# Kernel tuning notes

Measured on AMD Instinct MI355X. Metric: run time of the kernel, lower is better.

The kernel has to match this reference:

```python
import jax, jax.numpy as jnp
import numpy as np

PS = 32
EMBED_DIM = 768
IN_CH = 3
IMG = 1024
NUM_PATCHES = 992  # ini_row = i for H=1024, so need i+32 <= 1024
SPIKE_IDX = np.array([5, 300, 800])
SPIKE_VAL = 1.0e6  # makes val ~= 23.94 < 24 -> nearest size 16 -> subdivided


def _token_layout(iw_np, num_patches, ps, H):
    """Replicates the module's data-dependent patch-size / subpatch-position logic.
    Returns static (rows, cols, sizes) for every output token, in emission order."""
    avg = iw_np.mean()
    val = np.minimum(ps * avg ** 0.05 / iw_np ** 0.05, float(ps))
    choices = np.array([32, 16, 8, 4], dtype=np.float64)  # argmin picks first on tie, like min(list)
    sizes = choices[np.argmin(np.abs(val[:, None] - choices[None, :]), axis=1)].astype(np.int64)
    rows, cols, szs = [], [], []
    for i in range(num_patches):
        ini_col = (i * ps) % H
        ini_row = (i * ps * ps) // H
        s = int(sizes[i])
        if 3 < s < ps:
            ns = ps // s  # num_subpatches; subpatch_size == s
            for j in range(ns):
                rows.append(ini_row + (j * s) // ns)
                cols.append(ini_col + (j * s) % (ns * s))
                szs.append(s)
        else:
            rows.append(ini_row)
            cols.append(ini_col)
            szs.append(ps)
    return np.asarray(rows), np.asarray(cols), np.asarray(szs)


def _embed(x, W, b, rows, cols, szs, ps):
    E, C = W.shape[0], W.shape[1]
    B = x.shape[0]
    T = szs.shape[0]
    out = jnp.zeros((B, T, E), dtype=x.dtype)
    for s in np.unique(szs):
        s = int(s)
        idx = np.nonzero(szs == s)[0]  # static token slots for this size group
        r, c = rows[idx], cols[idx]
        if s == ps:
            Wf = W
        else:
            kd = ps // s  # fold the ps x ps kernel down to s x s, as in the module
            Wf = W.reshape(E, C, kd, kd, s, s).sum(axis=(2, 3))
        ar = np.arange(s)
        # gather [B, C, K, s, s] sub-patches with static advanced indexing
        patches = x[:, :, r[:, None, None] + ar[None, :, None], c[:, None, None] + ar[None, None, :]]
        tok = jnp.einsum('bckhw,echw->bke', patches, Wf) + b  # stride==kernel -> 1 token each
        out = out.at[:, jnp.asarray(idx), :].set(tok)
    return out


def setup_inputs() -> dict:
    key = jax.random.key(0)
    k_x, k_w, k_iw, k_b = jax.random.split(key, 4)
    x = jax.random.normal(k_x, (8, IN_CH, IMG, IMG), dtype=jnp.float32)
    iw = jax.random.uniform(k_iw, (1, NUM_PATCHES), dtype=jnp.float32, minval=0.5, maxval=1.5)
    iw = iw.at[0, SPIKE_IDX].set(SPIKE_VAL)  # 3 high-importance patches -> size-16 subdivision
    W = jax.random.normal(k_w, (EMBED_DIM, IN_CH, PS, PS), dtype=jnp.float32) * 0.02
    b = jax.random.normal(k_b, (EMBED_DIM,), dtype=jnp.float32) * 0.02
    return {"x": x, "importance_weights": iw, "W": W, "b": b, "num_patches": NUM_PATCHES}


def reference(x, importance_weights, W, b, num_patches):
    iw = np.asarray(importance_weights)[0]
    rows, cols, szs = _token_layout(iw, int(num_patches), PS, x.shape[3])
    return _embed(x, W, b, rows, cols, szs, PS)  # [B, T, E]
```

## Files before the change

### kernel.cpp

```cpp
#include <hip/hip_runtime.h>


typedef __attribute__((ext_vector_type(8))) short bf16x8;
typedef __attribute__((ext_vector_type(4))) float f32x4;

#define K_DIM 3072
#define N_DIM 768

__device__ __forceinline__ unsigned short f2bf(float f) {
  unsigned int u = __float_as_uint(f);
  u += 0x7fffu + ((u >> 16) & 1u);
  return (unsigned short)(u >> 16);
}

__device__ __forceinline__ void gload16(const void* g, void* l) {
  __builtin_amdgcn_global_load_lds(
      (const __attribute__((address_space(1))) void*)g,
      (__attribute__((address_space(3))) void*)l, 16, 0, 0);
}

__global__ __launch_bounds__(1024)
void prep_kernel(const float* __restrict__ W, unsigned short* __restrict__ Wb, int w4,
                 const float* __restrict__ iw, int P,
                 int* __restrict__ tokBase, int* __restrict__ tokMask, int NB_W) {
  int bid = blockIdx.x;
  int tid = threadIdx.x;
  if (bid < NB_W) {
    int idx = bid * 1024 + tid;
    if (idx < w4) {
      float4 f = *(const float4*)(W + (size_t)idx * 4);
      ushort4 o;
      o.x = f2bf(f.x); o.y = f2bf(f.y); o.z = f2bf(f.z); o.w = f2bf(f.w);
      *(ushort4*)(Wb + (size_t)idx * 4) = o;
    }
    return;
  }
  __shared__ double s_wsum[16];
  __shared__ double s_avg;
  __shared__ int s_cnt[1024];
  float v = (tid < P) ? iw[tid] : 0.0f;
  double d = (double)v;
#pragma unroll
  for (int off = 32; off > 0; off >>= 1) d += __shfl_down(d, off, 64);
  if ((tid & 63) == 0) s_wsum[tid >> 6] = d;
  __syncthreads();
  if (tid == 0) {
    double s = 0.0;
    for (int i = 0; i < 16; ++i) s += s_wsum[i];
    s_avg = s / (double)P;
  }
  __syncthreads();
  int cnt = 0, sz = 32;
  if (tid < P) {
    double val = 32.0 * pow(s_avg / (double)v, 0.05);
    if (val > 32.0) val = 32.0;
    sz = (val >= 24.0) ? 32 : (val >= 12.0) ? 16 : (val >= 6.0) ? 8 : 4;
    cnt = (sz < 32) ? (32 / sz) : 1;
  }
  s_cnt[tid] = cnt;
  __syncthreads();
  for (int dl = 1; dl < 1024; dl <<= 1) {
    int add = (tid >= dl) ? s_cnt[tid - dl] : 0;
    __syncthreads();
    s_cnt[tid] += add;
    __syncthreads();
  }
  if (tid < P) {
    int off = s_cnt[tid] - cnt;
    int ini_col = (tid * 32) & 1023;
    int ini_row = (tid * 32 * 32) >> 10;
    if (sz == 32) {
      tokBase[off] = ini_row * 1024 + ini_col;
      tokMask[off] = 31;
    } else {
      int ns = 32 / sz;
      for (int j = 0; j < ns; ++j) {
        int r = ini_row + (j * sz) / ns;
        int c = ini_col + ((j * sz) & 31);
        tokBase[off + j] = r * 1024 + c;
        tokMask[off + j] = sz - 1;
      }
    }
  }
}

__global__ __launch_bounds__(256)
void gather_kernel(const float* __restrict__ x,
                   const int* __restrict__ tokBase,
                   const int* __restrict__ tokMask,
                   unsigned short* __restrict__ Ab) {
  int t = blockIdx.x;
  int b = blockIdx.y;
  int T = gridDim.x;
  int m = b * T + t;
  int base = tokBase[t];
  int mask = tokMask[t];
  int sh = __popc(mask);
  const float* xb = x + (size_t)b * 3145728 + (size_t)base;
  unsigned short* arow = Ab + (size_t)m * K_DIM;
#pragma unroll
  for (int it = 0; it < 3; ++it) {
    int g = it * 256 + threadIdx.x;
    int p = g * 4;
    int c = p >> 10;
    int f = p & 1023;
    int h = (f >> sh) & mask;
    int w = f & mask;
    float4 fv = *(const float4*)(xb + (size_t)c * 1048576 + h * 1024 + w);
    ushort4 o;
    o.x = f2bf(fv.x); o.y = f2bf(fv.y); o.z = f2bf(fv.z); o.w = f2bf(fv.w);
    *(ushort4*)(arow + p) = o;
  }
}

__global__ __launch_bounds__(256, 2)
void gemm_kernel(const unsigned short* __restrict__ A, const unsigned short* __restrict__ Wb,
                 const float* __restrict__ bias, float* __restrict__ out, int Mtot) {
  __shared__ unsigned short lds[2][2][128 * 64];
  int tid = threadIdx.x;
  int lane = tid & 63;
  int wave = tid >> 6;
  int wr = wave >> 1, wc = wave & 1;
  int mBase = blockIdx.y * 128;
  int nBase = blockIdx.x * 128;

  f32x4 acc[4][4] = {};

  int lrow = lane >> 3;
  int schunk = (lane & 7) ^ lrow;
  const unsigned short* Ag = A + (size_t)(mBase + wave * 32 + lrow) * K_DIM + schunk * 8;
  const unsigned short* Bg = Wb + (size_t)(nBase + wave * 32 + lrow) * K_DIM + schunk * 8;
  unsigned short* Adst0 = &lds[0][0][(wave * 32) * 64] + lane * 8;
  unsigned short* Bdst0 = &lds[0][1][(wave * 32) * 64] + lane * 8;

#define STAGE(BUF, KOFF)                                                    \
  {                                                                         \
    _Pragma("unroll")                                                       \
    for (int inst = 0; inst < 4; ++inst) {                                  \
      gload16(Ag + (size_t)(inst * 8) * K_DIM + (KOFF),                     \
              Adst0 + (size_t)(BUF) * 2 * 8192 + inst * 512);               \
      gload16(Bg + (size_t)(inst * 8) * K_DIM + (KOFF),                     \
              Bdst0 + (size_t)(BUF) * 2 * 8192 + inst * 512);               \
    }                                                                       \
  }

  int rr = lane & 15, q = lane >> 4;
  int r7 = rr & 7;

#define COMPUTE(BUF)                                                        \
  {                                                                         \
    const unsigned short* Ab_ = &lds[BUF][0][0];                            \
    const unsigned short* Bb_ = &lds[BUF][1][0];                            \
    _Pragma("unroll")                                                       \
    for (int kh = 0; kh < 2; ++kh) {                                        \
      bf16x8 aF[4], bF[4];                                                  \
      _Pragma("unroll")                                                     \
      for (int i = 0; i < 4; ++i)                                           \
        aF[i] = *(const bf16x8*)&Ab_[(wr * 64 + i * 16 + rr) * 64 +         \
                                     ((kh * 4 + q) ^ r7) * 8];              \
      _Pragma("unroll")                                                     \
      for (int j = 0; j < 4; ++j)                                           \
        bF[j] = *(const bf16x8*)&Bb_[(wc * 64 + j * 16 + rr) * 64 +         \
                                     ((kh * 4 + q) ^ r7) * 8];              \
      _Pragma("unroll")                                                     \
      for (int i = 0; i < 4; ++i)                                           \
        _Pragma("unroll")                                                   \
        for (int j = 0; j < 4; ++j)                                         \
          acc[i][j] = __builtin_amdgcn_mfma_f32_16x16x32_bf16(aF[i], bF[j], \
                                                              acc[i][j], 0, 0, 0); \
    }                                                                       \
  }

  STAGE(0, 0)
  __syncthreads();
  int buf = 0;
  for (int k0 = 0; k0 < K_DIM; k0 += 64) {
    if (k0 + 64 < K_DIM) {
      if (buf == 0) STAGE(1, k0 + 64) else STAGE(0, k0 + 64)
    }
    if (buf == 0) COMPUTE(0) else COMPUTE(1)
    __syncthreads();
    buf ^= 1;
  }
#undef STAGE
#undef COMPUTE

#pragma unroll
  for (int j = 0; j < 4; ++j) {
    int n = nBase + wc * 64 + j * 16 + rr;
    float bv = bias[n];
#pragma unroll
    for (int i = 0; i < 4; ++i) {
      int mrow = mBase + wr * 64 + i * 16 + q * 4;
#pragma unroll
      for (int r2 = 0; r2 < 4; ++r2) {
        int m = mrow + r2;
        if (m < Mtot) out[(size_t)m * N_DIM + n] = acc[i][j][r2] + bv;
      }
    }
  }
}

extern "C" void kernel_launch(void* const* d_in, const int* in_sizes, int n_in,
                              void* d_out, int out_size, void* d_ws, size_t ws_size,
                              hipStream_t stream) {
  const float* x  = (const float*)d_in[0];
  const float* iw = (const float*)d_in[1];
  const float* W  = (const float*)d_in[2];
  const float* b  = (const float*)d_in[3];
  int P = in_sizes[1];
  int B = in_sizes[0] / (3 * 1024 * 1024);
  int E = in_sizes[3];
  int T = out_size / (B * E);
  int Mtot = B * T;
  int Mpad = (Mtot + 127) & ~127;

  char* ws = (char*)d_ws;
  int* tokBase = (int*)ws;
  int* tokMask = (int*)(ws + 32768);
  unsigned short* Wb = (unsigned short*)(ws + 65536);
  unsigned short* Ab = (unsigned short*)(ws + 65536 + (size_t)E * K_DIM * 2);

  int w4 = E * K_DIM / 4;
  int NB_W = (w4 + 1023) / 1024;
  prep_kernel<<<NB_W + 1, 1024, 0, stream>>>(W, Wb, w4, iw, P, tokBase, tokMask, NB_W);

  dim3 gGrid(T, B);
  gather_kernel<<<gGrid, 256, 0, stream>>>(x, tokBase, tokMask, Ab);


  dim3 grid(N_DIM / 128, Mpad / 128);
  gemm_kernel<<<grid, 256, 0, stream>>>(Ab, Wb, b, (float*)d_out, Mtot);
}
```

Measured before the change: 248.2 us.

## Use 128x64 GEMM tiles with XCD-aware block remapping and higher occupancy

The GEMM tile shrinks from 128x128 to 128x64, so the N dimension now has 12 tiles and the grid roughly doubles in size. The launch becomes a 1D grid whose block index is remapped so that neighbouring tiles land on the same XCD, which should improve L2 reuse of A rows. Launch bounds rise to 3 blocks per SM because LDS and accumulator use per block drop. The aim is to fill the GPU better, since Mtot is about 8k, at the cost of lower arithmetic intensity per tile and more redundant loads of A.

```diff
diff --git a/kernel.cpp b/kernel.cpp
--- a/kernel.cpp
+++ b/kernel.cpp
@@ -113,35 +113,43 @@
   }
 }
 
-__global__ __launch_bounds__(256, 2)
+__global__ __launch_bounds__(256, 3)
 void gemm_kernel(const unsigned short* __restrict__ A, const unsigned short* __restrict__ Wb,
                  const float* __restrict__ bias, float* __restrict__ out, int Mtot) {
-  __shared__ unsigned short lds[2][2][128 * 64];
+  __shared__ unsigned short lds[2][12288];
   int tid = threadIdx.x;
   int lane = tid & 63;
   int wave = tid >> 6;
   int wr = wave >> 1, wc = wave & 1;
-  int mBase = blockIdx.y * 128;
-  int nBase = blockIdx.x * 128;
-
-  f32x4 acc[4][4] = {};
+
+  int lin = blockIdx.x;
+  int nwg = gridDim.x;
+  int q8 = nwg >> 3, r8 = nwg & 7;
+  int xcd = lin & 7, slot = lin >> 3;
+  int wg = (xcd < r8) ? xcd * (q8 + 1) + slot
+                      : r8 * (q8 + 1) + (xcd - r8) * q8 + slot;
+  int mBase = (wg / 12) * 128;
+  int nBase = (wg % 12) * 64;
+
+  f32x4 acc[4][2] = {};
 
   int lrow = lane >> 3;
   int schunk = (lane & 7) ^ lrow;
   const unsigned short* Ag = A + (size_t)(mBase + wave * 32 + lrow) * K_DIM + schunk * 8;
-  const unsigned short* Bg = Wb + (size_t)(nBase + wave * 32 + lrow) * K_DIM + schunk * 8;
-  unsigned short* Adst0 = &lds[0][0][(wave * 32) * 64] + lane * 8;
-  unsigned short* Bdst0 = &lds[0][1][(wave * 32) * 64] + lane * 8;
+  const unsigned short* Bg = Wb + (size_t)(nBase + wave * 16 + lrow) * K_DIM + schunk * 8;
+  unsigned short* Adst0 = &lds[0][(wave * 32) * 64] + lane * 8;
+  unsigned short* Bdst0 = &lds[0][8192 + (wave * 16) * 64] + lane * 8;
 
 #define STAGE(BUF, KOFF)                                                    \
   {                                                                         \
     _Pragma("unroll")                                                       \
-    for (int inst = 0; inst < 4; ++inst) {                                  \
+    for (int inst = 0; inst < 4; ++inst)                                    \
       gload16(Ag + (size_t)(inst * 8) * K_DIM + (KOFF),                     \
-              Adst0 + (size_t)(BUF) * 2 * 8192 + inst * 512);               \
+              Adst0 + (size_t)(BUF) * 12288 + inst * 512);                  \
+    _Pragma("unroll")                                                       \
+    for (int inst = 0; inst < 2; ++inst)                                    \
       gload16(Bg + (size_t)(inst * 8) * K_DIM + (KOFF),                     \
-              Bdst0 + (size_t)(BUF) * 2 * 8192 + inst * 512);               \
-    }                                                                       \
+              Bdst0 + (size_t)(BUF) * 12288 + inst * 512);                  \
   }
 
   int rr = lane & 15, q = lane >> 4;
@@ -149,23 +157,23 @@
 
 #define COMPUTE(BUF)                                                        \
   {                                                                         \
-    const unsigned short* Ab_ = &lds[BUF][0][0];                            \
-    const unsigned short* Bb_ = &lds[BUF][1][0];                            \
+    const unsigned short* A_ = &lds[BUF][0];                                \
+    const unsigned short* B_ = &lds[BUF][8192];                             \
     _Pragma("unroll")                                                       \
     for (int kh = 0; kh < 2; ++kh) {                                        \
-      bf16x8 aF[4], bF[4];                                                  \
+      bf16x8 aF[4], bF[2];                                                  \
       _Pragma("unroll")                                                     \
       for (int i = 0; i < 4; ++i)                                           \
-        aF[i] = *(const bf16x8*)&Ab_[(wr * 64 + i * 16 + rr) * 64 +         \
-                                     ((kh * 4 + q) ^ r7) * 8];              \
+        aF[i] = *(const bf16x8*)&A_[(wr * 64 + i * 16 + rr) * 64 +          \
+                                    ((kh * 4 + q) ^ r7) * 8];               \
       _Pragma("unroll")                                                     \
-      for (int j = 0; j < 4; ++j)                                           \
-        bF[j] = *(const bf16x8*)&Bb_[(wc * 64 + j * 16 + rr) * 64 +         \
-                                     ((kh * 4 + q) ^ r7) * 8];              \
+      for (int j = 0; j < 2; ++j)                                           \
+        bF[j] = *(const bf16x8*)&B_[(wc * 32 + j * 16 + rr) * 64 +          \
+                                    ((kh * 4 + q) ^ r7) * 8];               \
       _Pragma("unroll")                                                     \
       for (int i = 0; i < 4; ++i)                                           \
         _Pragma("unroll")                                                   \
-        for (int j = 0; j < 4; ++j)                                         \
+        for (int j = 0; j < 2; ++j)                                         \
           acc[i][j] = __builtin_amdgcn_mfma_f32_16x16x32_bf16(aF[i], bF[j], \
                                                               acc[i][j], 0, 0, 0); \
     }                                                                       \
@@ -186,8 +194,8 @@
 #undef COMPUTE
 
 #pragma unroll
-  for (int j = 0; j < 4; ++j) {
-    int n = nBase + wc * 64 + j * 16 + rr;
+  for (int j = 0; j < 2; ++j) {
+    int n = nBase + wc * 32 + j * 16 + rr;
     float bv = bias[n];
 #pragma unroll
     for (int i = 0; i < 4; ++i) {
@@ -229,6 +237,6 @@
   gather_kernel<<<gGrid, 256, 0, stream>>>(x, tokBase, tokMask, Ab);
 
 
-  dim3 grid(N_DIM / 128, Mpad / 128);
+  dim3 grid((N_DIM / 64) * (Mpad / 128));
   gemm_kernel<<<grid, 256, 0, stream>>>(Ab, Wb, b, (float*)d_out, Mtot);
 }
```

Result: faster. 240.2 us (-3.2%).
